# Optimization experiments

Measured on AMD Instinct MI355X. Metric: run time of the kernel, lower is better.

## Reference

```python
import jax, jax.numpy as jnp
import numpy as np

N, D, M = 262144, 64, 256
CLAMP = -1e-9  # clamp_max value for the ray denominator


def setup_inputs() -> dict:
    key = jax.random.key(0)
    kz, kp, ka, kb = jax.random.split(key, 4)
    return {
        "z": jax.random.normal(kz, (N, D), dtype=jnp.float32),
        "pivot": jax.random.normal(kp, (D,), dtype=jnp.float32),
        "At": jax.random.normal(ka, (D, M), dtype=jnp.float32),
        "b": jax.random.normal(kb, (M,), dtype=jnp.float32),
    }


def reference(z, pivot, At, b):
    # sign_arg: [N, M] — signed constraint violation A z - b
    sign_arg = z @ At - b[None, :]
    ind = sign_arg >= 0  # violated constraints
    ray = pivot[None, :] - z  # [N, D] direction toward the interior pivot
    # denominator clamped to <= -1e-9 and detached (constant w.r.t. grads)
    denom = jax.lax.stop_gradient(jnp.minimum(ray @ At, CLAMP))  # [N, M]
    alpha = -sign_arg / denom
    # step size = max over violated constraints (alpha*ind zeros out satisfied ones)
    common_alpha = jnp.max(alpha * ind.astype(alpha.dtype), axis=1)  # [N]
    common_ind = jnp.any(ind, axis=1)  # [N] — move only if some constraint violated
    return z + common_ind[:, None].astype(z.dtype) * (common_alpha[:, None] * ray)
```

## Files before the change

### kernel.cpp

```cpp
#include <hip/hip_runtime.h>

#define DIMK 64
#define MC 256
#define BR 64
#define NROWS 262144
#define NT (NROWS / BR)
#define PBLK 512
#define TPB (NT / PBLK)

#define WS_AT 1024
#define WS_NEED (1024 + 65536)

#define LDS_GMP 65536
#define LDS_FP_SIZE (65536 + 2048)

#define LDS_AH 0
#define LDS_AL 16384
#define LDS_GM 32768

typedef _Float16 half8 __attribute__((ext_vector_type(8)));
typedef float f32x16 __attribute__((ext_vector_type(16)));

__device__ __forceinline__ void cvt_half8(const float* v, half8& h, half8& l) {
#pragma unroll
    for (int j = 0; j < 8; ++j) {
        h[j] = (_Float16)v[j];
        l[j] = (_Float16)(v[j] - (float)h[j]);
    }
}

__global__ void precompute_c(const float* __restrict__ pivot,
                             const float* __restrict__ At,
                             float* __restrict__ ws) {
    const int t = threadIdx.x;
    float acc = 0.f;
#pragma unroll
    for (int k = 0; k < DIMK; ++k) acc = fmaf(pivot[k], At[k * MC + t], acc);
    ws[t] = acc;
}

__global__ void precompute_at(const float* __restrict__ pivot,
                              const float* __restrict__ At,
                              float* __restrict__ ws) {
    const int t = threadIdx.x;
    float col[DIMK];
    float acc = 0.f;
#pragma unroll
    for (int k = 0; k < DIMK; ++k) {
        col[k] = At[k * MC + t];
        acc = fmaf(pivot[k], col[k], acc);
    }
    ws[t] = acc;
    char* wsb = (char*)ws + WS_AT;
#pragma unroll
    for (int s = 0; s < 2; ++s) {
#pragma unroll
        for (int kc = 0; kc < 4; ++kc) {
            half8 h, l;
#pragma unroll
            for (int j = 0; j < 8; ++j) {
                const float v = col[s * 32 + kc * 8 + j];
                h[j] = (_Float16)v;
                l[j] = (_Float16)(v - (float)h[j]);
            }
            const int off = ((s * 4 + kc) * 256 + t) * 16;
            *(half8*)(wsb + off) = h;
            *(half8*)(wsb + off + 32768) = l;
        }
    }
}

__global__ __launch_bounds__(512, 4)
void fused_constrain_p(const float* __restrict__ z,
                       const float* __restrict__ pivot,
                       const float* __restrict__ b,
                       const float* __restrict__ ws,
                       float* __restrict__ out) {
    extern __shared__ __align__(16) char lds[];

    const int tid  = threadIdx.x;
    const int lane = tid & 63;
    const int li   = lane & 31;
    const int hi   = lane >> 5;
    const int wid  = tid >> 6;
    const int rg   = wid >> 2;
    const int cg   = wid & 3;
    const int R0   = rg * 32;
    const int colbase = cg * 64;

    float bv[2], cv[2];
#pragma unroll
    for (int ct = 0; ct < 2; ++ct) {
        const int c = colbase + ct * 32 + li;
        bv[ct] = b[c];
        cv[ct] = ws[c];
    }
    const float2 p2 = *(const float2*)(pivot + 2 * li);

    float4 zfA[4];
    {
        const float* zr = z + blockIdx.x * (TPB * BR * DIMK) +
                          (R0 + li) * DIMK + hi * 8;
        zfA[0] = *(const float4*)(zr);
        zfA[1] = *(const float4*)(zr + 4);
        zfA[2] = *(const float4*)(zr + 16);
        zfA[3] = *(const float4*)(zr + 20);
    }

    {
        const char* wsA = (const char*)ws + WS_AT;
#pragma unroll
        for (int p = 0; p < 8; ++p) {
            const int f = p * 512 + tid;
            *(float4*)(lds + f * 16) = *(const float4*)(wsA + f * 16);
        }
    }
    __syncthreads();

    const int Bbase = hi * 4096 + (colbase + li) * 16;

    auto tile_body = [&](float4 (&zc)[4], float4 (&zn)[4],
                         const int i, const bool pf) {
        const int tbase = (blockIdx.x * TPB + i) * (BR * DIMK);
        const float* zr = z + tbase + (R0 + li) * DIMK + hi * 8;

        float4 zs1[4];
        zs1[0] = *(const float4*)(zr + 32);
        zs1[1] = *(const float4*)(zr + 36);
        zs1[2] = *(const float4*)(zr + 48);
        zs1[3] = *(const float4*)(zr + 52);
        if (pf) {
            const float* zp = zr + BR * DIMK;
            zn[0] = *(const float4*)(zp);
            zn[1] = *(const float4*)(zp + 4);
            zn[2] = *(const float4*)(zp + 16);
            zn[3] = *(const float4*)(zp + 20);
        }

        f32x16 acc[2];
#pragma unroll
        for (int ct = 0; ct < 2; ++ct)
#pragma unroll
            for (int e = 0; e < 16; ++e) acc[ct][e] = 0.f;

        half8 azh[2], azl[2];

        auto mfma_step = [&](const int sOff) {
#pragma unroll
            for (int ksl = 0; ksl < 2; ++ksl) {
                const int ob = Bbase + sOff + ksl * 8192;
                const half8 ah = azh[ksl], al = azl[ksl];
#pragma unroll
                for (int ct = 0; ct < 2; ++ct) {
                    const half8 bh = *(const half8*)(lds + ob + ct * 512);
                    const half8 bl = *(const half8*)(lds + ob + ct * 512 + 32768);
                    acc[ct] = __builtin_amdgcn_mfma_f32_32x32x16_f16(ah, bh, acc[ct], 0, 0, 0);
                    acc[ct] = __builtin_amdgcn_mfma_f32_32x32x16_f16(ah, bl, acc[ct], 0, 0, 0);
                    acc[ct] = __builtin_amdgcn_mfma_f32_32x32x16_f16(al, bh, acc[ct], 0, 0, 0);
                }
            }
        };

        cvt_half8((const float*)zc, azh[0], azl[0]);
        cvt_half8((const float*)zc + 8, azh[1], azl[1]);
        mfma_step(0);
        cvt_half8((const float*)zs1, azh[0], azl[0]);
        cvt_half8((const float*)zs1 + 8, azh[1], azl[1]);
        mfma_step(16384);

        float gm[16];
#pragma unroll
        for (int r = 0; r < 16; ++r) gm[r] = 0.f;
#pragma unroll
        for (int ct = 0; ct < 2; ++ct)
#pragma unroll
            for (int r = 0; r < 16; ++r) {
                const float sv = acc[ct][r];
                const float sa = sv - bv[ct];
                const float qd = fmaxf(sv - cv[ct], 1e-9f);
                gm[r] = fmaxf(gm[r], sa * __builtin_amdgcn_rcpf(qd));
            }
#pragma unroll
        for (int r = 0; r < 16; ++r)
#pragma unroll
            for (int off = 1; off < 32; off <<= 1)
                gm[r] = fmaxf(gm[r], __shfl_xor(gm[r], off));

        float* gmb = (float*)(lds + LDS_GMP + ((i & 1) << 10));
#pragma unroll
        for (int r = 0; r < 16; ++r) {
            const int row = (r & 3) + 8 * (r >> 2) + 4 * hi;
            if (li == 0) gmb[((rg << 5) + row) * 4 + cg] = gm[r];
        }
        __syncthreads();

#pragma unroll
        for (int rr = 0; rr < 4; ++rr) {
            const int r   = cg * 4 + rr;
            const int row = (r & 3) + 8 * (r >> 2) + 4 * hi;
            const float* g4 = &gmb[((rg << 5) + row) * 4];
            const float g = fmaxf(fmaxf(g4[0], g4[1]), fmaxf(g4[2], g4[3]));
            const int idx = tbase + (R0 + row) * DIMK + 2 * li;
            const float2 zz = *(const float2*)(z + idx);
            float2 o;
            o.x = fmaf(g, p2.x - zz.x, zz.x);
            o.y = fmaf(g, p2.y - zz.y, zz.y);
            *(float2*)(out + idx) = o;
        }
    };

    float4 zfB[4];
#pragma clang loop unroll(disable)
    for (int j = 0; j < TPB / 2; ++j) {
        tile_body(zfA, zfB, 2 * j, true);
        tile_body(zfB, zfA, 2 * j + 1, j < TPB / 2 - 1);
    }
}

__global__ __launch_bounds__(256, 4)
void fused_constrain_fb(const float* __restrict__ z,
                        const float* __restrict__ pivot,
                        const float* __restrict__ At,
                        const float* __restrict__ b,
                        const float* __restrict__ ws,
                        float* __restrict__ out) {
    __shared__ __align__(16) char lds[33280];

    const int tid  = threadIdx.x;
    const int lane = tid & 63;
    const int li   = lane & 31;
    const int hi   = lane >> 5;
    const int wid  = tid >> 6;
    const int rg   = wid >> 1;
    const int cg   = wid & 1;
    const int R0   = rg * 32;
    const int colbase = cg * 128;
    const int base = blockIdx.x * (BR * DIMK);

    float4 zf[8];
    {
        const float* zr = z + base + (R0 + li) * DIMK + hi * 8;
#pragma unroll
        for (int q = 0; q < 4; ++q) {
            const float* p = zr + (q >> 1) * 32 + (q & 1) * 16;
            zf[q * 2 + 0] = *(const float4*)(p);
            zf[q * 2 + 1] = *(const float4*)(p + 4);
        }
    }
    const int swzT = (tid & 3) ^ ((tid >> 2) & 3);
#pragma unroll
    for (int kc = 0; kc < 4; ++kc) {
        float v[8];
#pragma unroll
        for (int j = 0; j < 8; ++j) v[j] = At[(kc * 8 + j) * MC + tid];
        half8 h, l;
#pragma unroll
        for (int j = 0; j < 8; ++j) {
            h[j] = (_Float16)v[j];
            l[j] = (_Float16)(v[j] - (float)h[j]);
        }
        const int off = tid * 64 + ((kc ^ swzT) << 4);
        *(half8*)(lds + LDS_AH + off) = h;
        *(half8*)(lds + LDS_AL + off) = l;
    }

    half8 azh[4], azl[4];
    const float* zv = (const float*)zf;
#pragma unroll
    for (int q = 0; q < 4; ++q)
        cvt_half8(zv + q * 8, azh[q], azl[q]);

    f32x16 acc[4];
#pragma unroll
    for (int ct = 0; ct < 4; ++ct)
#pragma unroll
        for (int e = 0; e < 16; ++e) acc[ct][e] = 0.f;

    const int swz = (li & 3) ^ ((li >> 2) & 3);
    __syncthreads();
#pragma unroll
    for (int ksl = 0; ksl < 2; ++ksl) {
        const int cb = ((ksl * 2 + hi) ^ swz) << 4;
        const half8 ah = azh[ksl], al = azl[ksl];
#pragma unroll
        for (int ct = 0; ct < 4; ++ct) {
            const int off = (colbase + ct * 32 + li) * 64 + cb;
            const half8 bh = *(const half8*)(lds + LDS_AH + off);
            const half8 bl = *(const half8*)(lds + LDS_AL + off);
            acc[ct] = __builtin_amdgcn_mfma_f32_32x32x16_f16(ah, bh, acc[ct], 0, 0, 0);
            acc[ct] = __builtin_amdgcn_mfma_f32_32x32x16_f16(ah, bl, acc[ct], 0, 0, 0);
            acc[ct] = __builtin_amdgcn_mfma_f32_32x32x16_f16(al, bh, acc[ct], 0, 0, 0);
        }
    }
    __syncthreads();
#pragma unroll
    for (int kc = 0; kc < 4; ++kc) {
        float v[8];
#pragma unroll
        for (int j = 0; j < 8; ++j) v[j] = At[(32 + kc * 8 + j) * MC + tid];
        half8 h, l;
#pragma unroll
        for (int j = 0; j < 8; ++j) {
            h[j] = (_Float16)v[j];
            l[j] = (_Float16)(v[j] - (float)h[j]);
        }
        const int off = tid * 64 + ((kc ^ swzT) << 4);
        *(half8*)(lds + LDS_AH + off) = h;
        *(half8*)(lds + LDS_AL + off) = l;
    }
    __syncthreads();
#pragma unroll
    for (int ksl = 0; ksl < 2; ++ksl) {
        const int cb = ((ksl * 2 + hi) ^ swz) << 4;
        const half8 ah = azh[2 + ksl], al = azl[2 + ksl];
#pragma unroll
        for (int ct = 0; ct < 4; ++ct) {
            const int off = (colbase + ct * 32 + li) * 64 + cb;
            const half8 bh = *(const half8*)(lds + LDS_AH + off);
            const half8 bl = *(const half8*)(lds + LDS_AL + off);
            acc[ct] = __builtin_amdgcn_mfma_f32_32x32x16_f16(ah, bh, acc[ct], 0, 0, 0);
            acc[ct] = __builtin_amdgcn_mfma_f32_32x32x16_f16(ah, bl, acc[ct], 0, 0, 0);
            acc[ct] = __builtin_amdgcn_mfma_f32_32x32x16_f16(al, bh, acc[ct], 0, 0, 0);
        }
    }

    float bv[4], cv[4];
#pragma unroll
    for (int ct = 0; ct < 4; ++ct) {
        const int c = colbase + ct * 32 + li;
        bv[ct] = b[c];
        cv[ct] = ws[c];
    }
    float gm[16];
#pragma unroll
    for (int r = 0; r < 16; ++r) gm[r] = 0.f;
#pragma unroll
    for (int ct = 0; ct < 4; ++ct)
#pragma unroll
        for (int r = 0; r < 16; ++r) {
            const float sv = acc[ct][r];
            const float sa = sv - bv[ct];
            const float qd = fmaxf(sv - cv[ct], 1e-9f);
            gm[r] = fmaxf(gm[r], sa * __builtin_amdgcn_rcpf(qd));
        }
#pragma unroll
    for (int r = 0; r < 16; ++r)
#pragma unroll
        for (int off = 1; off < 32; off <<= 1)
            gm[r] = fmaxf(gm[r], __shfl_xor(gm[r], off));

    float* gmbuf = (float*)(lds + LDS_GM);
#pragma unroll
    for (int r = 0; r < 16; ++r) {
        const int row = (r & 3) + 8 * (r >> 2) + 4 * hi;
        if (li == 0) gmbuf[rg * 64 + row * 2 + cg] = gm[r];
    }
    __syncthreads();

    const float2 p2 = *(const float2*)(pivot + 2 * li);
    const int r0 = cg * 8;
#pragma unroll
    for (int rr = 0; rr < 8; ++rr) {
        const int r   = r0 + rr;
        const int row = (r & 3) + 8 * (r >> 2) + 4 * hi;
        const float g = fmaxf(gm[r], gmbuf[rg * 64 + row * 2 + (cg ^ 1)]);
        const int idx = base + (R0 + row) * DIMK + 2 * li;
        const float2 zz = *(const float2*)(z + idx);
        float2 o;
        o.x = fmaf(g, p2.x - zz.x, zz.x);
        o.y = fmaf(g, p2.y - zz.y, zz.y);
        *(float2*)(out + idx) = o;
    }
}

extern "C" void kernel_launch(void* const* d_in, const int* in_sizes, int n_in,
                              void* d_out, int out_size, void* d_ws, size_t ws_size,
                              hipStream_t stream) {
    const float* z     = (const float*)d_in[0];
    const float* pivot = (const float*)d_in[1];
    const float* At    = (const float*)d_in[2];
    const float* b     = (const float*)d_in[3];
    float* ws = (float*)d_ws;
    if (ws_size >= (size_t)WS_NEED) {
        precompute_at<<<dim3(1), dim3(MC), 0, stream>>>(pivot, At, ws);
        fused_constrain_p<<<dim3(PBLK), dim3(512), LDS_FP_SIZE, stream>>>(
            z, pivot, b, ws, (float*)d_out);
    } else {
        precompute_c<<<dim3(1), dim3(MC), 0, stream>>>(pivot, At, ws);
        fused_constrain_fb<<<dim3(NT), dim3(256), 0, stream>>>(
            z, pivot, At, b, ws, (float*)d_out);
    }
}
```

Baseline: 158.2 us.

## Split fused kernel into GEMM row-max pass and separate elementwise apply pass

The fused persistent kernel is replaced by two kernels. The first has each wave own whole 32-row strips across all 256 columns, so there is no cross-wave LDS reduction or per-tile __syncthreads, and it writes one per-row step size to workspace. The second streams z again with vectorized float4 loads and nontemporal stores to apply the update. This removes intra-block synchronization and lets the apply pass run at full bandwidth, at the cost of reading z a second time from memory, an extra launch, and a larger workspace requirement.

```diff
diff --git a/kernel.cpp b/kernel.cpp
--- a/kernel.cpp
+++ b/kernel.cpp
@@ -2,17 +2,17 @@
 
 #define DIMK 64
 #define MC 256
-#define BR 64
 #define NROWS 262144
-#define NT (NROWS / BR)
-#define PBLK 512
-#define TPB (NT / PBLK)
+#define NSTRIPS (NROWS / 32)
+#define K1B 512
+#define K1W 4
+#define K1I (NSTRIPS / (K1B * K1W))
+#define K2B 2048
+#define K2IT (NROWS * DIMK / 4 / (K2B * 256))
 
 #define WS_AT 1024
-#define WS_NEED (1024 + 65536)
-
-#define LDS_GMP 65536
-#define LDS_FP_SIZE (65536 + 2048)
+#define WS_GM (WS_AT + 65536)
+#define WS_NEED_SPLIT (WS_GM + NROWS * 4)
 
 #define LDS_AH 0
 #define LDS_AL 16384
@@ -20,6 +20,7 @@
 
 typedef _Float16 half8 __attribute__((ext_vector_type(8)));
 typedef float f32x16 __attribute__((ext_vector_type(16)));
+typedef float f32x4 __attribute__((ext_vector_type(4)));
 
 __device__ __forceinline__ void cvt_half8(const float* v, half8& h, half8& l) {
 #pragma unroll
@@ -70,109 +71,83 @@
     }
 }
 
-__global__ __launch_bounds__(512, 4)
-void fused_constrain_p(const float* __restrict__ z,
-                       const float* __restrict__ pivot,
-                       const float* __restrict__ b,
-                       const float* __restrict__ ws,
-                       float* __restrict__ out) {
-    extern __shared__ __align__(16) char lds[];
+__global__ __launch_bounds__(256, 2)
+void k1_gemm_rowmax(const float* __restrict__ z,
+                    const float* __restrict__ b,
+                    const float* __restrict__ ws,
+                    float* __restrict__ gmv) {
+    __shared__ __align__(16) char lds[65536];
 
     const int tid  = threadIdx.x;
     const int lane = tid & 63;
     const int li   = lane & 31;
     const int hi   = lane >> 5;
     const int wid  = tid >> 6;
-    const int rg   = wid >> 2;
-    const int cg   = wid & 3;
-    const int R0   = rg * 32;
-    const int colbase = cg * 64;
-
-    float bv[2], cv[2];
-#pragma unroll
-    for (int ct = 0; ct < 2; ++ct) {
-        const int c = colbase + ct * 32 + li;
-        bv[ct] = b[c];
-        cv[ct] = ws[c];
-    }
-    const float2 p2 = *(const float2*)(pivot + 2 * li);
-
-    float4 zfA[4];
-    {
-        const float* zr = z + blockIdx.x * (TPB * BR * DIMK) +
-                          (R0 + li) * DIMK + hi * 8;
-        zfA[0] = *(const float4*)(zr);
-        zfA[1] = *(const float4*)(zr + 4);
-        zfA[2] = *(const float4*)(zr + 16);
-        zfA[3] = *(const float4*)(zr + 20);
-    }
 
     {
         const char* wsA = (const char*)ws + WS_AT;
 #pragma unroll
-        for (int p = 0; p < 8; ++p) {
-            const int f = p * 512 + tid;
+        for (int p = 0; p < 16; ++p) {
+            const int f = p * 256 + tid;
             *(float4*)(lds + f * 16) = *(const float4*)(wsA + f * 16);
         }
     }
-    __syncthreads();
-
-    const int Bbase = hi * 4096 + (colbase + li) * 16;
-
-    auto tile_body = [&](float4 (&zc)[4], float4 (&zn)[4],
-                         const int i, const bool pf) {
-        const int tbase = (blockIdx.x * TPB + i) * (BR * DIMK);
-        const float* zr = z + tbase + (R0 + li) * DIMK + hi * 8;
-
-        float4 zs1[4];
-        zs1[0] = *(const float4*)(zr + 32);
-        zs1[1] = *(const float4*)(zr + 36);
-        zs1[2] = *(const float4*)(zr + 48);
-        zs1[3] = *(const float4*)(zr + 52);
-        if (pf) {
-            const float* zp = zr + BR * DIMK;
-            zn[0] = *(const float4*)(zp);
-            zn[1] = *(const float4*)(zp + 4);
-            zn[2] = *(const float4*)(zp + 16);
-            zn[3] = *(const float4*)(zp + 20);
-        }
-
-        f32x16 acc[2];
-#pragma unroll
-        for (int ct = 0; ct < 2; ++ct)
+    float bv[8], cv[8];
+#pragma unroll
+    for (int ct = 0; ct < 8; ++ct) {
+        bv[ct] = b[ct * 32 + li];
+        cv[ct] = ws[ct * 32 + li];
+    }
+    __syncthreads();
+
+    auto zload = [&](float4 (&zb)[8], const int strip) {
+        const float* zr = z + (strip * 32 + li) * DIMK + hi * 8;
+        zb[0] = *(const float4*)(zr);      zb[1] = *(const float4*)(zr + 4);
+        zb[2] = *(const float4*)(zr + 16); zb[3] = *(const float4*)(zr + 20);
+        zb[4] = *(const float4*)(zr + 32); zb[5] = *(const float4*)(zr + 36);
+        zb[6] = *(const float4*)(zr + 48); zb[7] = *(const float4*)(zr + 52);
+    };
+
+    float4 zb[8];
+    zload(zb, blockIdx.x * (K1W * K1I) + wid);
+
+#pragma unroll
+    for (int it = 0; it < K1I; ++it) {
+        const int strip = blockIdx.x * (K1W * K1I) + it * K1W + wid;
+
+        half8 azh[4], azl[4];
+#pragma unroll
+        for (int q = 0; q < 4; ++q)
+            cvt_half8((const float*)&zb[q * 2], azh[q], azl[q]);
+
+        if (it < K1I - 1) zload(zb, strip + K1W);
+
+        f32x16 acc[8];
+#pragma unroll
+        for (int ct = 0; ct < 8; ++ct)
 #pragma unroll
             for (int e = 0; e < 16; ++e) acc[ct][e] = 0.f;
 
-        half8 azh[2], azl[2];
-
-        auto mfma_step = [&](const int sOff) {
-#pragma unroll
-            for (int ksl = 0; ksl < 2; ++ksl) {
-                const int ob = Bbase + sOff + ksl * 8192;
-                const half8 ah = azh[ksl], al = azl[ksl];
-#pragma unroll
-                for (int ct = 0; ct < 2; ++ct) {
-                    const half8 bh = *(const half8*)(lds + ob + ct * 512);
-                    const half8 bl = *(const half8*)(lds + ob + ct * 512 + 32768);
-                    acc[ct] = __builtin_amdgcn_mfma_f32_32x32x16_f16(ah, bh, acc[ct], 0, 0, 0);
-                    acc[ct] = __builtin_amdgcn_mfma_f32_32x32x16_f16(ah, bl, acc[ct], 0, 0, 0);
-                    acc[ct] = __builtin_amdgcn_mfma_f32_32x32x16_f16(al, bh, acc[ct], 0, 0, 0);
-                }
+#pragma unroll
+        for (int st = 0; st < 4; ++st) {
+            const int ob = (st >> 1) * 16384 + (st & 1) * 8192 +
+                           hi * 4096 + li * 16;
+            const half8 ah = azh[st], al = azl[st];
+#pragma unroll
+            for (int ct = 0; ct < 8; ++ct) {
+                const half8 bh = *(const half8*)(lds + ob + ct * 512);
+                const half8 bl = *(const half8*)(lds + ob + ct * 512 + 32768);
+                acc[ct] = __builtin_amdgcn_mfma_f32_32x32x16_f16(ah, bh, acc[ct], 0, 0, 0);
+                acc[ct] = __builtin_amdgcn_mfma_f32_32x32x16_f16(ah, bl, acc[ct], 0, 0, 0);
+                acc[ct] = __builtin_amdgcn_mfma_f32_32x32x16_f16(al, bh, acc[ct], 0, 0, 0);
             }
-        };
-
-        cvt_half8((const float*)zc, azh[0], azl[0]);
-        cvt_half8((const float*)zc + 8, azh[1], azl[1]);
-        mfma_step(0);
-        cvt_half8((const float*)zs1, azh[0], azl[0]);
-        cvt_half8((const float*)zs1 + 8, azh[1], azl[1]);
-        mfma_step(16384);
+        }
 
         float gm[16];
 #pragma unroll
         for (int r = 0; r < 16; ++r) gm[r] = 0.f;
 #pragma unroll
-        for (int ct = 0; ct < 2; ++ct)
+        for (int ct = 0; ct < 8; ++ct)
 #pragma unroll
             for (int r = 0; r < 16; ++r) {
                 const float sv = acc[ct][r];
@@ -186,34 +161,34 @@
             for (int off = 1; off < 32; off <<= 1)
                 gm[r] = fmaxf(gm[r], __shfl_xor(gm[r], off));
 
-        float* gmb = (float*)(lds + LDS_GMP + ((i & 1) << 10));
-#pragma unroll
-        for (int r = 0; r < 16; ++r) {
-            const int row = (r & 3) + 8 * (r >> 2) + 4 * hi;
-            if (li == 0) gmb[((rg << 5) + row) * 4 + cg] = gm[r];
-        }
-        __syncthreads();
-
-#pragma unroll
-        for (int rr = 0; rr < 4; ++rr) {
-            const int r   = cg * 4 + rr;
-            const int row = (r & 3) + 8 * (r >> 2) + 4 * hi;
-            const float* g4 = &gmb[((rg << 5) + row) * 4];
-            const float g = fmaxf(fmaxf(g4[0], g4[1]), fmaxf(g4[2], g4[3]));
-            const int idx = tbase + (R0 + row) * DIMK + 2 * li;
-            const float2 zz = *(const float2*)(z + idx);
-            float2 o;
-            o.x = fmaf(g, p2.x - zz.x, zz.x);
-            o.y = fmaf(g, p2.y - zz.y, zz.y);
-            *(float2*)(out + idx) = o;
-        }
-    };
-
-    float4 zfB[4];
-#pragma clang loop unroll(disable)
-    for (int j = 0; j < TPB / 2; ++j) {
-        tile_body(zfA, zfB, 2 * j, true);
-        tile_body(zfB, zfA, 2 * j + 1, j < TPB / 2 - 1);
+        if (li == 0) {
+#pragma unroll
+            for (int r = 0; r < 16; ++r) {
+                const int row = (r & 3) + 8 * (r >> 2) + 4 * hi;
+                gmv[strip * 32 + row] = gm[r];
+            }
+        }
+    }
+}
+
+__global__ __launch_bounds__(256)
+void k2_apply(const float* __restrict__ z,
+              const float* __restrict__ pivot,
+              const float* __restrict__ gmv,
+              float* __restrict__ out) {
+    const int t = blockIdx.x * 256 + threadIdx.x;
+    const f32x4 pv = ((const f32x4*)pivot)[t & 15];
+#pragma unroll
+    for (int it = 0; it < K2IT; ++it) {
+        const int i = t + it * (K2B * 256);
+        const float g = gmv[i >> 4];
+        const f32x4 z4 = ((const f32x4*)z)[i];
+        f32x4 o;
+        o.x = fmaf(g, pv.x - z4.x, z4.x);
+        o.y = fmaf(g, pv.y - z4.y, z4.y);
+        o.z = fmaf(g, pv.z - z4.z, z4.z);
+        o.w = fmaf(g, pv.w - z4.w, z4.w);
+        __builtin_nontemporal_store(o, &((f32x4*)out)[i]);
     }
 }
 
@@ -235,7 +210,7 @@
     const int cg   = wid & 1;
     const int R0   = rg * 32;
     const int colbase = cg * 128;
-    const int base = blockIdx.x * (BR * DIMK);
+    const int base = blockIdx.x * (64 * DIMK);
 
     float4 zf[8];
     {
@@ -381,13 +356,15 @@
     const float* At    = (const float*)d_in[2];
     const float* b     = (const float*)d_in[3];
     float* ws = (float*)d_ws;
-    if (ws_size >= (size_t)WS_NEED) {
+    if (ws_size >= (size_t)WS_NEED_SPLIT) {
+        float* gmv = (float*)((char*)d_ws + WS_GM);
         precompute_at<<<dim3(1), dim3(MC), 0, stream>>>(pivot, At, ws);
-        fused_constrain_p<<<dim3(PBLK), dim3(512), LDS_FP_SIZE, stream>>>(
-            z, pivot, b, ws, (float*)d_out);
+        k1_gemm_rowmax<<<dim3(K1B), dim3(256), 0, stream>>>(z, b, ws, gmv);
+        k2_apply<<<dim3(K2B), dim3(256), 0, stream>>>(z, pivot, gmv,
+                                                      (float*)d_out);
     } else {
         precompute_c<<<dim3(1), dim3(MC), 0, stream>>>(pivot, At, ws);
-        fused_constrain_fb<<<dim3(NT), dim3(256), 0, stream>>>(
+        fused_constrain_fb<<<dim3(NROWS / 64), dim3(256), 0, stream>>>(
             z, pivot, At, b, ws, (float*)d_out);
     }
 }
```

Result: slower. 168.7 us (+6.6%).
